# Kernel optimization log

Measured on AMD Instinct MI355X. Metric: run time of the kernel, lower is better.

The kernel has to match this reference:

```python
import jax, jax.numpy as jnp
import numpy as np

B, P, D = 64, 256, 768
S = P + 1            # class token + patches
GRID = 16.0          # sqrt(no_of_patches)
N_IMGS = 10000


def setup_inputs() -> dict:
    key = jax.random.key(0)
    ks = jax.random.split(key, 10)
    sc = 1.0 / np.sqrt(D)
    return {
        "x": jax.random.normal(ks[0], (B, S, D), jnp.float32),
        "img_ids": jax.random.randint(ks[1], (B,), 0, N_IMGS),
        "mask": jnp.ones((B, S), jnp.int32),
        "avgs": 0.1 * jax.random.normal(ks[2], (N_IMGS, 2, P), jnp.float32),
        "std_devs": jnp.ones((N_IMGS, 2, P), jnp.float32),
        "Wq": sc * jax.random.normal(ks[3], (D, D), jnp.float32),
        "bq": jnp.zeros((D,), jnp.float32),
        "Wk": sc * jax.random.normal(ks[4], (D, D), jnp.float32),
        "bk": jnp.zeros((D,), jnp.float32),
        "Wv": sc * jax.random.normal(ks[5], (D, D), jnp.float32),
        "bv": jnp.zeros((D,), jnp.float32),
        "noise_x": jax.random.normal(ks[6], (B, P), jnp.float32),  # torch.normal(0, sigma)
        "noise_y": jax.random.normal(ks[7], (B, P), jnp.float32),
    }


def reference(x, img_ids, mask, avgs, std_devs, Wq, bq, Wk, bk, Wv, bv, noise_x, noise_y):
    # nn.Linear: y = x @ W^T + b
    q = jnp.einsum("bsd,ed->bse", x, Wq) + bq  # (B,S,D)
    k = jnp.einsum("bsd,ed->bse", x, Wk) + bk
    v = jnp.einsum("bsd,ed->bse", x, Wv) + bv

    a = avgs[img_ids]       # (B,2,P)
    sd = std_devs[img_ids]  # (B,2,P)
    half = (GRID - 1.0) / 2.0
    kx = half * (1.0 + jnp.tanh((noise_x + a[:, 0]) * sd[:, 0]))  # (B,P) in (0, GRID-1)
    ky = half * (1.0 + jnp.tanh((noise_y + a[:, 1]) * sd[:, 1]))
    kx1, kx2 = jnp.ceil(kx), jnp.floor(kx)
    ky1, ky2 = jnp.ceil(ky), jnp.floor(ky)

    # corner order matches original: (x1,y1), (x2,y1), (x1,y2), (x2,y2)
    cx = jnp.stack([kx1, kx2, kx1, kx2], axis=1)  # (B,4,P)
    cy = jnp.stack([ky1, ky1, ky2, ky2], axis=1)
    idxs = jax.lax.stop_gradient(GRID * cy + cx).astype(jnp.int32)  # (B,4,P), < P

    sk = jnp.take_along_axis(k[:, None], idxs[..., None], axis=2)  # (B,4,P,D)
    sv = jnp.take_along_axis(v[:, None], idxs[..., None], axis=2)
    cls = jnp.ones((B, 4, 1, D), sk.dtype)
    skf = jnp.concatenate([cls, sk], axis=2)  # (B,4,S,D)
    svf = jnp.concatenate([cls, sv], axis=2)

    # score per query s against its 4 sampled corner keys; softmax over the 4 corners
    scores = jnp.einsum("bnsd,bsd->bsn", skf, q)   # (B,S,4)
    attn = jax.nn.softmax(scores, axis=-1)          # (B,S,4)
    attn_v = attn.transpose(0, 2, 1)[..., None] * svf  # (B,4,S,D)

    # bilinear weights (1-|cx-kx|)*(1-|cy-ky|); class-token weight fixed to 1
    w = (1.0 - jnp.abs(cx - kx[:, None])) * (1.0 - jnp.abs(cy - ky[:, None]))  # (B,4,P)
    wf = jnp.concatenate([jnp.ones((B, 4, 1), w.dtype), w], axis=2)  # (B,4,S)
    out = jnp.einsum("bns,bnsd->bsd", wf, attn_v)  # (B,S,D)
    return out
```

## Files before the change

kernel.cpp:

```cpp
#include <hip/hip_runtime.h>
#include <math.h>


typedef _Float16 f16x8 __attribute__((ext_vector_type(8)));
typedef _Float16 f16x4 __attribute__((ext_vector_type(4)));
typedef float    f32x4 __attribute__((ext_vector_type(4)));

#define MTOT 16448
#define DD   768
#define NC   2304
#define XCH (129*24*512)
#define WCH (18*24*512)

__global__ __launch_bounds__(256) void prepass(
    const float* __restrict__ x,
    const float* __restrict__ Wq, const float* __restrict__ Wk, const float* __restrict__ Wv,
    _Float16* __restrict__ xp, _Float16* __restrict__ wp)
{
    const int gidx = blockIdx.x * 256 + threadIdx.x;
    const float* src;
    _Float16* dst;
    if (gidx < XCH) {
        const int c = gidx & 511, kk = (gidx >> 9) % 24, t = gidx / 12288;
        const int row = ((c >> 6) << 4) + (c & 15);
        int gm = t * 128 + row; gm = gm < MTOT ? gm : MTOT - 1;
        src = x + (size_t)gm * DD + kk * 32 + ((c >> 4) & 3) * 8;
        dst = xp + (size_t)gidx * 8;
    } else {
        const int g = gidx - XCH;
        const int c = g & 511, kk = (g >> 9) % 24, t = g / 12288;
        const int wrow = t * 128 + ((c >> 6) << 4) + (c & 15);
        const float* W = wrow < 768 ? Wq : (wrow < 1536 ? Wk : Wv);
        const int srow = wrow < 768 ? wrow : (wrow < 1536 ? wrow - 768 : wrow - 1536);
        src = W + (size_t)srow * DD + kk * 32 + ((c >> 4) & 3) * 8;
        dst = wp + (size_t)g * 8;
    }
    const float4 a = *(const float4*)src;
    const float4 b = *(const float4*)(src + 4);
    f16x8 o;
    o[0] = (_Float16)a.x; o[1] = (_Float16)a.y; o[2] = (_Float16)a.z; o[3] = (_Float16)a.w;
    o[4] = (_Float16)b.x; o[5] = (_Float16)b.y; o[6] = (_Float16)b.z; o[7] = (_Float16)b.w;
    *(f16x8*)dst = o;
}

__global__ __launch_bounds__(256) void qkv_gemm(
    const _Float16* __restrict__ xp, const _Float16* __restrict__ wp,
    const float* __restrict__ bq, const float* __restrict__ bk, const float* __restrict__ bv,
    _Float16* __restrict__ qkv)
{
    __shared__ __align__(16) _Float16 Ax[512 * 8];
    __shared__ __align__(16) _Float16 Bx[512 * 8];

    const int bid = blockIdx.x;
    const int xcd = bid & 7, pos = bid >> 3;
    const int q8 = 2322 / 8, r8 = 2322 % 8;
    const int orig = (xcd < r8) ? xcd * (q8 + 1) + pos
                                : r8 * (q8 + 1) + (xcd - r8) * q8 + pos;
    const int tileM = orig / 18, tileN = orig % 18;

    const int tid = threadIdx.x, lane = tid & 63, wid = tid >> 6;
    const int wm = wid >> 1, wn = wid & 1;
    const int r16 = lane & 15, kq = lane >> 4;

    const f32x4 zero = {0.f, 0.f, 0.f, 0.f};
    f32x4 acc[4][4];
    #pragma unroll
    for (int i = 0; i < 4; ++i)
        #pragma unroll
        for (int j = 0; j < 4; ++j) acc[i][j] = zero;

    const _Float16* Asrc = xp + (size_t)tileM * 24 * 512 * 8;
    const _Float16* Bsrc = wp + (size_t)tileN * 24 * 512 * 8;

    for (int kk = 0; kk < 24; ++kk) {
        __syncthreads();
        #pragma unroll
        for (int t = 0; t < 2; ++t) {
            const int c0 = t * 256 + wid * 64;
            __builtin_amdgcn_global_load_lds(
                (const __attribute__((address_space(1))) void*)(Asrc + ((size_t)(kk * 512 + c0 + lane)) * 8),
                (__attribute__((address_space(3))) void*)(&Ax[c0 * 8]), 16, 0, 0);
            __builtin_amdgcn_global_load_lds(
                (const __attribute__((address_space(1))) void*)(Bsrc + ((size_t)(kk * 512 + c0 + lane)) * 8),
                (__attribute__((address_space(3))) void*)(&Bx[c0 * 8]), 16, 0, 0);
        }
        __syncthreads();

        f16x8 a[4], b[4];
        #pragma unroll
        for (int i = 0; i < 4; ++i)
            a[i] = *(const f16x8*)(&Ax[((wm * 4 + i) * 64 + lane) * 8]);
        #pragma unroll
        for (int j = 0; j < 4; ++j)
            b[j] = *(const f16x8*)(&Bx[((wn * 4 + j) * 64 + lane) * 8]);
        #pragma unroll
        for (int i = 0; i < 4; ++i)
            #pragma unroll
            for (int j = 0; j < 4; ++j)
                acc[i][j] = __builtin_amdgcn_mfma_f32_16x16x32_f16(a[i], b[j], acc[i][j], 0, 0, 0);
    }

    const int sec = tileN / 6;
    const float* bias = sec == 0 ? bq : (sec == 1 ? bk : bv);
    const int bcol0 = (tileN % 6) * 128 + wn * 64;
    #pragma unroll
    for (int i = 0; i < 4; ++i) {
        const int row0 = tileM * 128 + wm * 64 + i * 16 + kq * 4;
        #pragma unroll
        for (int j = 0; j < 4; ++j) {
            const int col = tileN * 128 + wn * 64 + j * 16 + r16;
            const float bb = bias[bcol0 + j * 16 + r16];
            #pragma unroll
            for (int t = 0; t < 4; ++t) {
                const int row = row0 + t;
                if (row < MTOT)
                    qkv[(size_t)row * NC + col] = (_Float16)(acc[i][j][t] + bb);
            }
        }
    }
}

__global__ __launch_bounds__(256) void attn_gather(
    const _Float16* __restrict__ qkv,
    const int*   __restrict__ ids,
    const float* __restrict__ avgs,
    const float* __restrict__ stds,
    const float* __restrict__ nx,
    const float* __restrict__ ny,
    float* __restrict__ out)
{
    const int tid  = threadIdx.x;
    const int lane = tid & 63;
    const int gid  = blockIdx.x * 4 + (tid >> 6);
    const int b = gid / 257, s = gid % 257;
    float* orow = out + (size_t)gid * DD;

    if (s == 0) {
        const float4 one = make_float4(1.f, 1.f, 1.f, 1.f);
        #pragma unroll
        for (int j = 0; j < 3; ++j)
            *(float4*)(orow + 4 * lane + 256 * j) = one;
        return;
    }
    const int p   = s - 1;
    const int img = ids[b];
    const size_t ab = (size_t)img * 512 + p;
    const float a0 = avgs[ab], a1 = avgs[ab + 256];
    const float s0 = stds[ab], s1 = stds[ab + 256];
    const float kx = 7.5f * (1.f + tanhf((nx[b * 256 + p] + a0) * s0));
    const float ky = 7.5f * (1.f + tanhf((ny[b * 256 + p] + a1) * s1));
    const float kx1 = ceilf(kx), kx2 = floorf(kx);
    const float ky1 = ceilf(ky), ky2 = floorf(ky);
    const float cx[4] = {kx1, kx2, kx1, kx2};
    const float cy[4] = {ky1, ky1, ky2, ky2};
    int   idx[4];
    float w[4];
    #pragma unroll
    for (int n = 0; n < 4; ++n) {
        idx[n] = (int)(16.f * cy[n] + cx[n]);
        w[n]   = (1.f - fabsf(cx[n] - kx)) * (1.f - fabsf(cy[n] - ky));
    }

    const _Float16* qrow = qkv + (size_t)gid * NC;
    float qf[12];
    #pragma unroll
    for (int j = 0; j < 3; ++j) {
        const f16x4 v = *(const f16x4*)(qrow + lane * 4 + j * 256);
        qf[4 * j + 0] = (float)v[0]; qf[4 * j + 1] = (float)v[1];
        qf[4 * j + 2] = (float)v[2]; qf[4 * j + 3] = (float)v[3];
    }

    float sc[4];
    #pragma unroll
    for (int n = 0; n < 4; ++n) {
        const _Float16* krow = qkv + (size_t)(b * 257 + idx[n]) * NC + 768;
        float a = 0.f;
        #pragma unroll
        for (int j = 0; j < 3; ++j) {
            const f16x4 kv = *(const f16x4*)(krow + lane * 4 + j * 256);
            a += qf[4 * j + 0] * (float)kv[0] + qf[4 * j + 1] * (float)kv[1]
               + qf[4 * j + 2] * (float)kv[2] + qf[4 * j + 3] * (float)kv[3];
        }
        sc[n] = a;
    }
    #pragma unroll
    for (int n = 0; n < 4; ++n)
        for (int off = 32; off > 0; off >>= 1)
            sc[n] += __shfl_xor(sc[n], off);

    const float mx = fmaxf(fmaxf(sc[0], sc[1]), fmaxf(sc[2], sc[3]));
    const float e0 = expf(sc[0] - mx), e1 = expf(sc[1] - mx),
                e2 = expf(sc[2] - mx), e3 = expf(sc[3] - mx);
    const float inv = 1.f / (e0 + e1 + e2 + e3);
    const float coef[4] = {e0 * inv * w[0], e1 * inv * w[1], e2 * inv * w[2], e3 * inv * w[3]};

    const _Float16* vr0 = qkv + (size_t)(b * 257 + idx[0]) * NC + 1536;
    const _Float16* vr1 = qkv + (size_t)(b * 257 + idx[1]) * NC + 1536;
    const _Float16* vr2 = qkv + (size_t)(b * 257 + idx[2]) * NC + 1536;
    const _Float16* vr3 = qkv + (size_t)(b * 257 + idx[3]) * NC + 1536;
    #pragma unroll
    for (int j = 0; j < 3; ++j) {
        const int d = lane * 4 + j * 256;
        const f16x4 v0 = *(const f16x4*)(vr0 + d);
        const f16x4 v1 = *(const f16x4*)(vr1 + d);
        const f16x4 v2 = *(const f16x4*)(vr2 + d);
        const f16x4 v3 = *(const f16x4*)(vr3 + d);
        float4 o;
        o.x = coef[0] * (float)v0[0] + coef[1] * (float)v1[0] + coef[2] * (float)v2[0] + coef[3] * (float)v3[0];
        o.y = coef[0] * (float)v0[1] + coef[1] * (float)v1[1] + coef[2] * (float)v2[1] + coef[3] * (float)v3[1];
        o.z = coef[0] * (float)v0[2] + coef[1] * (float)v1[2] + coef[2] * (float)v2[2] + coef[3] * (float)v3[2];
        o.w = coef[0] * (float)v0[3] + coef[1] * (float)v1[3] + coef[2] * (float)v2[3] + coef[3] * (float)v3[3];
        *(float4*)(orow + d) = o;
    }
}

extern "C" void kernel_launch(void* const* d_in, const int* in_sizes, int n_in,
                              void* d_out, int out_size, void* d_ws, size_t ws_size,
                              hipStream_t stream) {
    const float* x    = (const float*)d_in[0];
    const int*   ids  = (const int*)  d_in[1];
    const float* avgs = (const float*)d_in[3];
    const float* stds = (const float*)d_in[4];
    const float* Wq   = (const float*)d_in[5];
    const float* bq   = (const float*)d_in[6];
    const float* Wk   = (const float*)d_in[7];
    const float* bk   = (const float*)d_in[8];
    const float* Wv   = (const float*)d_in[9];
    const float* bv   = (const float*)d_in[10];
    const float* nx   = (const float*)d_in[11];
    const float* ny   = (const float*)d_in[12];
    float* out = (float*)d_out;

    char* ws = (char*)d_ws;
    _Float16* qkv = (_Float16*)ws;
    _Float16* xp  = (_Float16*)(ws + 75792384);
    _Float16* wp  = (_Float16*)(ws + 75792384 + 25362432);

    prepass<<<(XCH + WCH) / 256, 256, 0, stream>>>(x, Wq, Wk, Wv, xp, wp);
    qkv_gemm<<<2322, 256, 0, stream>>>(xp, wp, bq, bk, bv, qkv);
    attn_gather<<<4112, 256, 0, stream>>>(qkv, ids, avgs, stds, nx, ny, out);
}
```

Before: 141.5 us.

## Double-buffer QKV GEMM LDS tiles with K=64 steps and swizzle gather blocks

The prepass now packs x and W in 64-wide K chunks (12 steps instead of 24). The GEMM uses double-buffered LDS, prefetching the next chunk with global_load_lds while the MFMAs run on the current one, and uses explicit waitcnt and barriers. This is meant to hide global-load latency and halve the number of sync rounds. The attention gather remaps block IDs across XCDs for better L2 locality. The cost is four times the LDS per block (64KB), which may lower occupancy.

```diff
diff --git a/kernel.cpp b/kernel.cpp
--- a/kernel.cpp
+++ b/kernel.cpp
@@ -9,8 +9,9 @@
 #define MTOT 16448
 #define DD   768
 #define NC   2304
-#define XCH (129*24*512)
-#define WCH (18*24*512)
+#define NT   12
+#define XU   (129*12*1024)
+#define WU   (18*12*1024)
 
 __global__ __launch_bounds__(256) void prepass(
     const float* __restrict__ x,
@@ -20,19 +21,23 @@
     const int gidx = blockIdx.x * 256 + threadIdx.x;
     const float* src;
     _Float16* dst;
-    if (gidx < XCH) {
-        const int c = gidx & 511, kk = (gidx >> 9) % 24, t = gidx / 12288;
-        const int row = ((c >> 6) << 4) + (c & 15);
-        int gm = t * 128 + row; gm = gm < MTOT ? gm : MTOT - 1;
-        src = x + (size_t)gm * DD + kk * 32 + ((c >> 4) & 3) * 8;
+    if (gidx < XU) {
+        const int u = gidx & 1023, k = (gidx >> 10) % NT, tile = gidx / (NT * 1024);
+        const int lane = u & 63, ksub = (u >> 6) & 1, mblk = u >> 7;
+        int row = tile * 128 + mblk * 16 + (lane & 15);
+        row = row < MTOT ? row : MTOT - 1;
+        const int col = k * 64 + ksub * 32 + (lane >> 4) * 8;
+        src = x + (size_t)row * DD + col;
         dst = xp + (size_t)gidx * 8;
     } else {
-        const int g = gidx - XCH;
-        const int c = g & 511, kk = (g >> 9) % 24, t = g / 12288;
-        const int wrow = t * 128 + ((c >> 6) << 4) + (c & 15);
+        const int g = gidx - XU;
+        const int u = g & 1023, k = (g >> 10) % NT, tile = g / (NT * 1024);
+        const int lane = u & 63, ksub = (u >> 6) & 1, mblk = u >> 7;
+        const int wrow = tile * 128 + mblk * 16 + (lane & 15);
         const float* W = wrow < 768 ? Wq : (wrow < 1536 ? Wk : Wv);
-        const int srow = wrow < 768 ? wrow : (wrow < 1536 ? wrow - 768 : wrow - 1536);
-        src = W + (size_t)srow * DD + kk * 32 + ((c >> 4) & 3) * 8;
+        const int srow = wrow - (wrow < 768 ? 0 : (wrow < 1536 ? 768 : 1536));
+        const int col = k * 64 + ksub * 32 + (lane >> 4) * 8;
+        src = W + (size_t)srow * DD + col;
         dst = wp + (size_t)g * 8;
     }
     const float4 a = *(const float4*)src;
@@ -48,8 +53,8 @@
     const float* __restrict__ bq, const float* __restrict__ bk, const float* __restrict__ bv,
     _Float16* __restrict__ qkv)
 {
-    __shared__ __align__(16) _Float16 Ax[512 * 8];
-    __shared__ __align__(16) _Float16 Bx[512 * 8];
+    __shared__ __align__(16) _Float16 Ax[2][8192];
+    __shared__ __align__(16) _Float16 Bx[2][8192];
 
     const int bid = blockIdx.x;
     const int xcd = bid & 7, pos = bid >> 3;
@@ -62,6 +67,9 @@
     const int wm = wid >> 1, wn = wid & 1;
     const int r16 = lane & 15, kq = lane >> 4;
 
+    const _Float16* Asrc = xp + (size_t)tileM * NT * 8192;
+    const _Float16* Bsrc = wp + (size_t)tileN * NT * 8192;
+
     const f32x4 zero = {0.f, 0.f, 0.f, 0.f};
     f32x4 acc[4][4];
     #pragma unroll
@@ -69,35 +77,57 @@
         #pragma unroll
         for (int j = 0; j < 4; ++j) acc[i][j] = zero;
 
-    const _Float16* Asrc = xp + (size_t)tileM * 24 * 512 * 8;
-    const _Float16* Bsrc = wp + (size_t)tileN * 24 * 512 * 8;
-
-    for (int kk = 0; kk < 24; ++kk) {
-        __syncthreads();
-        #pragma unroll
-        for (int t = 0; t < 2; ++t) {
-            const int c0 = t * 256 + wid * 64;
-            __builtin_amdgcn_global_load_lds(
-                (const __attribute__((address_space(1))) void*)(Asrc + ((size_t)(kk * 512 + c0 + lane)) * 8),
-                (__attribute__((address_space(3))) void*)(&Ax[c0 * 8]), 16, 0, 0);
-            __builtin_amdgcn_global_load_lds(
-                (const __attribute__((address_space(1))) void*)(Bsrc + ((size_t)(kk * 512 + c0 + lane)) * 8),
-                (__attribute__((address_space(3))) void*)(&Bx[c0 * 8]), 16, 0, 0);
-        }
-        __syncthreads();
-
-        f16x8 a[4], b[4];
-        #pragma unroll
-        for (int i = 0; i < 4; ++i)
-            a[i] = *(const f16x8*)(&Ax[((wm * 4 + i) * 64 + lane) * 8]);
-        #pragma unroll
-        for (int j = 0; j < 4; ++j)
-            b[j] = *(const f16x8*)(&Bx[((wn * 4 + j) * 64 + lane) * 8]);
-        #pragma unroll
-        for (int i = 0; i < 4; ++i)
+    #pragma unroll
+    for (int g = 0; g < 4; ++g) {
+        const int u = g * 256 + tid;
+        __builtin_amdgcn_global_load_lds(
+            (const __attribute__((address_space(1))) void*)(Asrc + (size_t)u * 8),
+            (__attribute__((address_space(3))) void*)(&Ax[0][u * 8]), 16, 0, 0);
+        __builtin_amdgcn_global_load_lds(
+            (const __attribute__((address_space(1))) void*)(Bsrc + (size_t)u * 8),
+            (__attribute__((address_space(3))) void*)(&Bx[0][u * 8]), 16, 0, 0);
+    }
+
+    for (int t = 0; t < NT; ++t) {
+        const int cur = t & 1;
+        if (t + 1 < NT) {
+            const size_t off = (size_t)(t + 1) * 8192;
+            #pragma unroll
+            for (int g = 0; g < 4; ++g) {
+                const int u = g * 256 + tid;
+                __builtin_amdgcn_global_load_lds(
+                    (const __attribute__((address_space(1))) void*)(Asrc + off + (size_t)u * 8),
+                    (__attribute__((address_space(3))) void*)(&Ax[cur ^ 1][u * 8]), 16, 0, 0);
+                __builtin_amdgcn_global_load_lds(
+                    (const __attribute__((address_space(1))) void*)(Bsrc + off + (size_t)u * 8),
+                    (__attribute__((address_space(3))) void*)(&Bx[cur ^ 1][u * 8]), 16, 0, 0);
+            }
+            asm volatile("s_waitcnt vmcnt(8)" ::: "memory");
+        } else {
+            asm volatile("s_waitcnt vmcnt(0)" ::: "memory");
+        }
+        __builtin_amdgcn_s_barrier();
+        __builtin_amdgcn_sched_barrier(0);
+
+        #pragma unroll
+        for (int s = 0; s < 2; ++s) {
+            f16x8 a[4], b[4];
+            #pragma unroll
+            for (int i = 0; i < 4; ++i)
+                a[i] = *(const f16x8*)(&Ax[cur][(((wm * 4 + i) * 2 + s) * 64 + lane) * 8]);
             #pragma unroll
             for (int j = 0; j < 4; ++j)
-                acc[i][j] = __builtin_amdgcn_mfma_f32_16x16x32_f16(a[i], b[j], acc[i][j], 0, 0, 0);
+                b[j] = *(const f16x8*)(&Bx[cur][(((wn * 4 + j) * 2 + s) * 64 + lane) * 8]);
+            #pragma unroll
+            for (int i = 0; i < 4; ++i)
+                #pragma unroll
+                for (int j = 0; j < 4; ++j)
+                    acc[i][j] = __builtin_amdgcn_mfma_f32_16x16x32_f16(a[i], b[j], acc[i][j], 0, 0, 0);
+        }
+        asm volatile("s_waitcnt lgkmcnt(0)" ::: "memory");
+        __builtin_amdgcn_sched_barrier(0);
+        __builtin_amdgcn_s_barrier();
+        __builtin_amdgcn_sched_barrier(0);
     }
 
     const int sec = tileN / 6;
@@ -131,7 +161,9 @@
 {
     const int tid  = threadIdx.x;
     const int lane = tid & 63;
-    const int gid  = blockIdx.x * 4 + (tid >> 6);
+    const int bid = blockIdx.x;
+    const int swz = (bid & 7) * 514 + (bid >> 3);
+    const int gid = swz * 4 + (tid >> 6);
     const int b = gid / 257, s = gid % 257;
     float* orow = out + (size_t)gid * DD;
 
@@ -236,7 +268,7 @@
     _Float16* xp  = (_Float16*)(ws + 75792384);
     _Float16* wp  = (_Float16*)(ws + 75792384 + 25362432);
 
-    prepass<<<(XCH + WCH) / 256, 256, 0, stream>>>(x, Wq, Wk, Wv, xp, wp);
+    prepass<<<(XU + WU) / 256, 256, 0, stream>>>(x, Wq, Wk, Wv, xp, wp);
     qkv_gemm<<<2322, 256, 0, stream>>>(xp, wp, bq, bk, bv, qkv);
     attn_gather<<<4112, 256, 0, stream>>>(qkv, ids, avgs, stds, nx, ny, out);
 }
```

Measured after the change: 133.3 us. 5.8% less time.
